# Performance work log

Measured on AMD Instinct MI355X. Metric: run time of the kernel, lower is better.

The kernel has to match this reference:

```python
import jax, jax.numpy as jnp
import numpy as np

B, S, DIM = 2, 4096, 2048
H, HK, HD = 16, 8, 128          # n_heads, n_kv_heads, head_dim
M = 128                          # FAVOR random features (== head_dim)
EPS_FAVOR = 1e-6
EPS_RMS = 1e-5


def _orthogonal_random_matrix(m, d, seed=0):
    # Gaussian orthogonal random features (Performer/FAVOR+), single square block.
    rng = np.random.default_rng(seed)
    a = rng.standard_normal((d, d)).astype(np.float32)
    q, _ = np.linalg.qr(a)
    mat = q.T[:m]
    row_norms = np.linalg.norm(rng.standard_normal((m, d)).astype(np.float32), axis=1)
    return jnp.asarray(mat * row_norms[:, None], dtype=jnp.float32)


def setup_inputs() -> dict:
    key = jax.random.key(0)
    ks = jax.random.split(key, 8)
    hidden_states = jax.random.normal(ks[0], (B, S, DIM), dtype=jnp.float32)
    attention_mask = jax.random.randint(ks[1], (B, S), 0, 2).astype(jnp.int32)
    ang = jax.random.uniform(ks[2], (B, S, HD // 2), dtype=jnp.float32,
                             minval=0.0, maxval=2.0 * np.pi)
    freqs_cis = jnp.stack([jnp.cos(ang), jnp.sin(ang)], axis=-1)  # (B,S,HD/2,2)
    sc = 0.02
    wq = sc * jax.random.normal(ks[3], (H * HD, DIM), dtype=jnp.float32)
    wk = sc * jax.random.normal(ks[4], (HK * HD, DIM), dtype=jnp.float32)
    wv = sc * jax.random.normal(ks[5], (HK * HD, DIM), dtype=jnp.float32)
    wo = sc * jax.random.normal(ks[6], (DIM, H * HD), dtype=jnp.float32)
    gq = jnp.ones((HD,), dtype=jnp.float32)
    gk = jnp.ones((HD,), dtype=jnp.float32)
    proj = _orthogonal_random_matrix(M, HD, seed=0)
    return {"hidden_states": hidden_states, "attention_mask": attention_mask,
            "freqs_cis": freqs_cis, "wq": wq, "wk": wk, "wv": wv, "wo": wo,
            "gq": gq, "gk": gk, "proj": proj}


def _rmsnorm(x, w):
    return x * jax.lax.rsqrt(jnp.mean(x * x, axis=-1, keepdims=True) + EPS_RMS) * w


def _rope(x, fc):
    # x: (B,S,Hx,HD), fc: (B,S,HD/2,2) as (cos, sin); complex mult on pairs.
    xr = x.reshape(*x.shape[:-1], HD // 2, 2)
    a, b = xr[..., 0], xr[..., 1]
    c = fc[:, :, None, :, 0]
    d = fc[:, :, None, :, 1]
    out = jnp.stack([a * c - b * d, a * d + b * c], axis=-1)
    return out.reshape(x.shape)


def _favor_features(x, proj, is_query):
    # x: (B,H,S,D), proj: (M,D) -> positive random features (B,H,S,M)
    d = x.shape[-1]
    x = x * (d ** -0.25)
    xp = jnp.einsum('bhsd,md->bhsm', x, proj)
    xp = xp - 0.5 * jnp.sum(x * x, axis=-1, keepdims=True)
    if is_query:
        xp = xp - jnp.max(xp, axis=-1, keepdims=True)
    else:
        xp = xp - jnp.max(xp, axis=2, keepdims=True)
    return jnp.exp(xp) * (M ** -0.5) + EPS_FAVOR


def reference(hidden_states, attention_mask, freqs_cis, wq, wk, wv, wo, gq, gk, proj):
    x = hidden_states
    q = jnp.einsum('bsd,od->bso', x, wq).reshape(B, S, H, HD)
    k = jnp.einsum('bsd,od->bso', x, wk).reshape(B, S, HK, HD)
    v = jnp.einsum('bsd,od->bso', x, wv).reshape(B, S, HK, HD)
    q = _rmsnorm(q, gq)
    k = _rmsnorm(k, gk)
    q = _rope(q, freqs_cis)
    k = _rope(k, freqs_cis)
    # GQA: expand kv heads (repeat_interleave along head dim)
    rep = H // HK
    k = jnp.repeat(k, rep, axis=2)
    v = jnp.repeat(v, rep, axis=2)
    # (B,H,S,D)
    qh = jnp.transpose(q, (0, 2, 1, 3))
    kh = jnp.transpose(k, (0, 2, 1, 3))
    vh = jnp.transpose(v, (0, 2, 1, 3))
    valid = (attention_mask > 0).astype(jnp.float32)[:, None, :, None]  # (B,1,S,1)
    q_phi = _favor_features(qh, proj, is_query=True)   # (B,H,S,M)
    k_phi = _favor_features(kh, proj, is_query=False)  # (B,H,S,M)
    k_phi = k_phi * valid
    vh = vh * valid
    kv = jnp.einsum('bhsm,bhsd->bhmd', k_phi, vh)      # (B,H,M,D)
    k_sum = jnp.sum(k_phi, axis=2)                     # (B,H,M)
    out = jnp.einsum('bhsm,bhmd->bhsd', q_phi, kv)
    denom = jnp.einsum('bhsm,bhm->bhs', q_phi, k_sum)[..., None]
    out = out / (denom + EPS_FAVOR)
    out = out * valid
    out = jnp.transpose(out, (0, 2, 1, 3)).reshape(B, S, H * HD)
    return jnp.einsum('bso,do->bsd', out, wo)


if __name__ == '__main__':
    o = reference(**setup_inputs())
    print(o.shape, o.dtype)
```

## Files before the change

### kernel.cpp

```cpp
#include <hip/hip_runtime.h>

#define B_ 2
#define S_ 4096
#define DIM_ 2048
#define H_ 16
#define HK_ 8
#define HD_ 128
#define M_ 128

typedef unsigned short u16;
typedef __bf16 bf16x8 __attribute__((ext_vector_type(8)));
typedef float f32x4 __attribute__((ext_vector_type(4)));

__device__ __forceinline__ u16 f2b(float f) {
  unsigned u = __float_as_uint(f);
  u = u + 0x7fffu + ((u >> 16) & 1u);
  return (u16)(u >> 16);
}
__device__ __forceinline__ float b2f(u16 h) {
  return __uint_as_float(((unsigned)h) << 16);
}
__device__ __forceinline__ unsigned fenc(float f) {
  unsigned u = __float_as_uint(f);
  return (u & 0x80000000u) ? ~u : (u | 0x80000000u);
}
__device__ __forceinline__ float fdec(unsigned e) {
  unsigned u = (e & 0x80000000u) ? (e & 0x7fffffffu) : ~e;
  return __uint_as_float(u);
}

__global__ void f2b_kernel(const float* __restrict__ in, u16* __restrict__ out, int n4) {
  int i = blockIdx.x * blockDim.x + threadIdx.x;
  if (i < n4) {
    float4 v = ((const float4*)in)[i];
    ushort4 o;
    o.x = f2b(v.x); o.y = f2b(v.y); o.z = f2b(v.z); o.w = f2b(v.w);
    ((ushort4*)out)[i] = o;
  }
}

__global__ void tproj_kernel(const float* __restrict__ p, float* __restrict__ pT) {
  int i = blockIdx.x * 256 + threadIdx.x;
  int d = i >> 7, m = i & 127;
  pT[i] = p[m * 128 + d];
}

__global__ void init_kernel(float* __restrict__ kvf, unsigned* __restrict__ kmaxu,
                            float* __restrict__ ksum) {
  int i = blockIdx.x * 256 + threadIdx.x;
  if (i < B_ * HK_ * M_ * HD_) kvf[i] = 0.f;
  if (i < B_ * HK_ * M_) { kmaxu[i] = 0u; ksum[i] = 0.f; }
}

__global__ __launch_bounds__(512, 2) void gemm256(
    const u16* __restrict__ A, const u16* __restrict__ Bm, float* __restrict__ C,
    int K, int ldc, int nbx)
{
  __shared__ __align__(16) u16 lds[65536];
  const int t = threadIdx.x;
  const int wave = t >> 6, lane = t & 63;
  const int nwg = gridDim.x;
  const int q8 = nwg >> 3;
  const int id = blockIdx.x;
  const int sid = (id & 7) * q8 + (id >> 3);
  const int nby = nwg / nbx;
  const int by = sid % nby;
  const int bx = sid / nby;
  const int wave_m = wave >> 2;
  const int wave_n = wave & 3;
  const int lr = lane & 15, lg = lane >> 4;

  const int srow = lane >> 3;
  const int scolE = (((lane & 7) ^ srow) << 3);

  const int NT = K >> 6;
  f32x4 acc[8][4] = {};

  const u16* Abase = A + (size_t)bx * 256 * (size_t)K;
  const u16* Bbase = Bm + (size_t)by * 256 * (size_t)K;

#define STAGE256(buf, k0)                                                            \
  {                                                                                  \
    _Pragma("unroll")                                                                \
    for (int sub = 0; sub < 2; sub++) {                                              \
      const int rowH = (wave * 2 + sub) * 8 + srow;                                  \
      const int chunk = (wave * 2 + sub) * 512;                                      \
      _Pragma("unroll")                                                              \
      for (int hh = 0; hh < 2; hh++) {                                               \
        __builtin_amdgcn_global_load_lds(                                            \
            (const __attribute__((address_space(1))) void*)(Abase + (size_t)(hh * 128 + rowH) * K + (k0) + scolE), \
            (__attribute__((address_space(3))) void*)&lds[(buf) * 16384 + hh * 8192 + chunk], 16, 0, 0); \
        __builtin_amdgcn_global_load_lds(                                            \
            (const __attribute__((address_space(1))) void*)(Bbase + (size_t)(hh * 128 + rowH) * K + (k0) + scolE), \
            (__attribute__((address_space(3))) void*)&lds[32768 + (buf) * 16384 + hh * 8192 + chunk], 16, 0, 0); \
      }                                                                              \
    }                                                                                \
  }

  STAGE256(0, 0);
  __syncthreads();

  for (int tt = 0; tt < NT; tt++) {
    const int cur = tt & 1;
    const int AbaseH = cur * 16384 + wave_m * 8192;
    const int BbaseH = 32768 + cur * 16384 + (wave_n >> 1) * 8192;
#pragma unroll
    for (int q = 0; q < 4; q++) {
      if (q == 0 && tt + 1 < NT) { STAGE256(cur ^ 1, (tt + 1) * 64) }
      const int mh = q >> 1, nh = q & 1;
      bf16x8 af[4][2], bfr[2][2];
#pragma unroll
      for (int m = 0; m < 4; m++) {
        const int r = mh * 64 + m * 16 + lr;
#pragma unroll
        for (int kk = 0; kk < 2; kk++) {
          const int cb = ((kk << 6) | (lg << 4)) ^ ((lr & 7) << 4);
          af[m][kk] = *(const bf16x8*)&lds[AbaseH + r * 64 + (cb >> 1)];
        }
      }
#pragma unroll
      for (int n = 0; n < 2; n++) {
        const int r = (wave_n & 1) * 64 + nh * 32 + n * 16 + lr;
#pragma unroll
        for (int kk = 0; kk < 2; kk++) {
          const int cb = ((kk << 6) | (lg << 4)) ^ ((lr & 7) << 4);
          bfr[n][kk] = *(const bf16x8*)&lds[BbaseH + r * 64 + (cb >> 1)];
        }
      }
      asm volatile("" ::: "memory");
      __builtin_amdgcn_s_barrier();
      asm volatile("" ::: "memory");
      __builtin_amdgcn_s_setprio(1);
#pragma unroll
      for (int kk = 0; kk < 2; kk++)
#pragma unroll
        for (int m = 0; m < 4; m++)
#pragma unroll
          for (int n = 0; n < 2; n++)
            acc[mh * 4 + m][nh * 2 + n] =
                __builtin_amdgcn_mfma_f32_16x16x32_bf16(af[m][kk], bfr[n][kk],
                                                        acc[mh * 4 + m][nh * 2 + n], 0, 0, 0);
      __builtin_amdgcn_s_setprio(0);
      asm volatile("" ::: "memory");
      if (q == 3) asm volatile("s_waitcnt vmcnt(0)" ::: "memory");
      __builtin_amdgcn_s_barrier();
      asm volatile("" ::: "memory");
    }
  }

  float* Cb = C + (size_t)(bx * 256 + wave_m * 128 + lg * 4) * ldc + by * 256 + wave_n * 64 + lr;
#pragma unroll
  for (int i = 0; i < 8; i++)
#pragma unroll
    for (int j = 0; j < 4; j++)
#pragma unroll
      for (int r = 0; r < 4; r++)
        Cb[(size_t)(i * 16 + r) * ldc + j * 16] = acc[i][j][r];
#undef STAGE256
}

__global__ __launch_bounds__(256) void gemm_bt(
    const u16* __restrict__ A, const u16* __restrict__ Bm, float* __restrict__ C,
    int M, int N, int K,
    unsigned long long sAb, unsigned long long sBb, unsigned long long sCb,
    int bshiftB, int ldc, int ksplit)
{
  __shared__ __align__(16) u16 sA[128 * 32];
  __shared__ __align__(16) u16 sB[128 * 32];
  const int t = threadIdx.x;
  const int wave = t >> 6, lane = t & 63;
  const int z = blockIdx.z;
  const int batch = z / ksplit;
  const int ks = z - batch * ksplit;
  const int kLen = K / ksplit, kBeg = ks * kLen;

  const u16* Ab = A + (size_t)batch * sAb + (size_t)blockIdx.x * 128 * (size_t)K;
  const u16* Bb = Bm + (size_t)(batch >> bshiftB) * sBb + (size_t)blockIdx.y * 128 * (size_t)K;
  float* Cb = C + (size_t)batch * sCb + (size_t)blockIdx.x * 128 * (size_t)ldc
                + (size_t)blockIdx.y * 128;

  const int r0 = wave * 16 + (lane >> 2);
  const int e0 = (lane & 3) * 8;
  const int wr = wave >> 1, wc = wave & 1;

  f32x4 acc[4][4] = {};

  for (int k0 = kBeg; k0 < kBeg + kLen; k0 += 32) {
#pragma unroll
    for (int i = 0; i < 2; i++) {
      __builtin_amdgcn_global_load_lds(
          (const __attribute__((address_space(1))) void*)(Ab + (size_t)(r0 + i * 64) * K + k0 + e0),
          (__attribute__((address_space(3))) void*)(&sA[(i * 4 + wave) * 512]), 16, 0, 0);
      __builtin_amdgcn_global_load_lds(
          (const __attribute__((address_space(1))) void*)(Bb + (size_t)(r0 + i * 64) * K + k0 + e0),
          (__attribute__((address_space(3))) void*)(&sB[(i * 4 + wave) * 512]), 16, 0, 0);
    }
    __syncthreads();
    bf16x8 av[4], bv[4];
#pragma unroll
    for (int m = 0; m < 4; m++)
      av[m] = *(const bf16x8*)&sA[(wr * 64 + m * 16 + (lane & 15)) * 32 + (lane >> 4) * 8];
#pragma unroll
    for (int n = 0; n < 4; n++)
      bv[n] = *(const bf16x8*)&sB[(wc * 64 + n * 16 + (lane & 15)) * 32 + (lane >> 4) * 8];
#pragma unroll
    for (int m = 0; m < 4; m++)
#pragma unroll
      for (int n = 0; n < 4; n++)
        acc[m][n] = __builtin_amdgcn_mfma_f32_16x16x32_bf16(av[m], bv[n], acc[m][n], 0, 0, 0);
    __syncthreads();
  }

  const int crow0 = wr * 64 + (lane >> 4) * 4;
  const int ccol = wc * 64 + (lane & 15);
  if (ksplit == 1) {
#pragma unroll
    for (int m = 0; m < 4; m++)
#pragma unroll
      for (int n = 0; n < 4; n++)
#pragma unroll
        for (int r = 0; r < 4; r++)
          Cb[(size_t)(crow0 + m * 16 + r) * ldc + ccol + n * 16] = acc[m][n][r];
  } else {
#pragma unroll
    for (int m = 0; m < 4; m++)
#pragma unroll
      for (int n = 0; n < 4; n++)
#pragma unroll
        for (int r = 0; r < 4; r++)
          atomicAdd(&Cb[(size_t)(crow0 + m * 16 + r) * ldc + ccol + n * 16], acc[m][n][r]);
  }
}

__global__ __launch_bounds__(256) void gemm_out_epi(
    const u16* __restrict__ qphib, const u16* __restrict__ kvb,
    const float* __restrict__ denom, const int* __restrict__ amask,
    u16* __restrict__ attnb)
{
  __shared__ __align__(16) u16 sA[128 * 32];
  __shared__ __align__(16) u16 sB[128 * 32];
  const int t = threadIdx.x;
  const int wave = t >> 6, lane = t & 63;
  const int batch = blockIdx.z;
  const int b = batch >> 4, h = batch & 15;

  const u16* Ab = qphib + (size_t)batch * 524288 + (size_t)blockIdx.x * 128 * 128;
  const u16* Bb = kvb + (size_t)(batch >> 1) * 16384;

  const int r0 = wave * 16 + (lane >> 2);
  const int e0 = (lane & 3) * 8;
  const int wr = wave >> 1, wc = wave & 1;

  f32x4 acc[4][4] = {};

  for (int k0 = 0; k0 < 128; k0 += 32) {
#pragma unroll
    for (int i = 0; i < 2; i++) {
      __builtin_amdgcn_global_load_lds(
          (const __attribute__((address_space(1))) void*)(Ab + (size_t)(r0 + i * 64) * 128 + k0 + e0),
          (__attribute__((address_space(3))) void*)(&sA[(i * 4 + wave) * 512]), 16, 0, 0);
      __builtin_amdgcn_global_load_lds(
          (const __attribute__((address_space(1))) void*)(Bb + (size_t)(r0 + i * 64) * 128 + k0 + e0),
          (__attribute__((address_space(3))) void*)(&sB[(i * 4 + wave) * 512]), 16, 0, 0);
    }
    __syncthreads();
    bf16x8 av[4], bv[4];
#pragma unroll
    for (int m = 0; m < 4; m++)
      av[m] = *(const bf16x8*)&sA[(wr * 64 + m * 16 + (lane & 15)) * 32 + (lane >> 4) * 8];
#pragma unroll
    for (int n = 0; n < 4; n++)
      bv[n] = *(const bf16x8*)&sB[(wc * 64 + n * 16 + (lane & 15)) * 32 + (lane >> 4) * 8];
#pragma unroll
    for (int m = 0; m < 4; m++)
#pragma unroll
      for (int n = 0; n < 4; n++)
        acc[m][n] = __builtin_amdgcn_mfma_f32_16x16x32_bf16(av[m], bv[n], acc[m][n], 0, 0, 0);
    __syncthreads();
  }

  const int crow0 = wr * 64 + (lane >> 4) * 4;
  const int ccol = wc * 64 + (lane & 15);
#pragma unroll
  for (int m = 0; m < 4; m++)
#pragma unroll
    for (int r = 0; r < 4; r++) {
      const int s = blockIdx.x * 128 + crow0 + m * 16 + r;
      const float inv = (amask[b * S_ + s] > 0)
                          ? 1.f / (denom[(size_t)batch * S_ + s] + 1e-6f) : 0.f;
      u16* orow = attnb + ((size_t)(b * S_ + s)) * 2048 + h * 128 + ccol;
#pragma unroll
      for (int n = 0; n < 4; n++)
        orow[n * 16] = f2b(acc[m][n][r] * inv);
    }
}

template <int IS_Q>
__global__ __launch_bounds__(256) void favor_kernel(
    const float* __restrict__ qkv, const float* __restrict__ fc,
    const float* __restrict__ g, const float* __restrict__ pT,
    float* __restrict__ kpre, unsigned* __restrict__ kmaxu,
    u16* __restrict__ qphib, const float* __restrict__ ksum, float* __restrict__ denom,
    int colbase)
{
  const int b = blockIdx.z, h = blockIdx.y;
  const int wave = threadIdx.x >> 6, lane = threadIdx.x & 63;
  const int s0 = blockIdx.x * 16 + wave * 4;
  __shared__ float xs[4][4][128];
  __shared__ float sm[4][128];
  float halfss[4];
  const int col = colbase + h * HD_;

#pragma unroll
  for (int tt = 0; tt < 4; tt++) {
    const int s = s0 + tt;
    const size_t row = (size_t)b * S_ + s;
    const float* xr = qkv + row * 4096 + col;
    float a = xr[2 * lane], bb = xr[2 * lane + 1];
    float ss = a * a + bb * bb;
#pragma unroll
    for (int o = 1; o < 64; o <<= 1) ss += __shfl_xor(ss, o);
    const float sc = rsqrtf(ss * (1.f / HD_) + 1e-5f);
    a *= sc * g[2 * lane];
    bb *= sc * g[2 * lane + 1];
    const float2 cs = *(const float2*)&fc[(row * 64 + lane) * 2];
    float na = a * cs.x - bb * cs.y;
    float nb = a * cs.y + bb * cs.x;
    na *= 0.29730177875068026f;
    nb *= 0.29730177875068026f;
    xs[wave][tt][2 * lane] = na;
    xs[wave][tt][2 * lane + 1] = nb;
    float s2 = na * na + nb * nb;
#pragma unroll
    for (int o = 1; o < 64; o <<= 1) s2 += __shfl_xor(s2, o);
    halfss[tt] = 0.5f * s2;
  }

  float acc[4][2] = {};
  for (int d = 0; d < 128; d++) {
    const float2 p = *(const float2*)&pT[d * 128 + 2 * lane];
#pragma unroll
    for (int tt = 0; tt < 4; tt++) {
      const float xv = xs[wave][tt][d];
      acc[tt][0] = fmaf(p.x, xv, acc[tt][0]);
      acc[tt][1] = fmaf(p.y, xv, acc[tt][1]);
    }
  }

  if (IS_Q) {
#pragma unroll
    for (int tt = 0; tt < 4; tt++) {
      const int s = s0 + tt;
      const float p0 = acc[tt][0] - halfss[tt], p1 = acc[tt][1] - halfss[tt];
      float mx = fmaxf(p0, p1);
#pragma unroll
      for (int o = 1; o < 64; o <<= 1) mx = fmaxf(mx, __shfl_xor(mx, o));
      const float f0 = expf(p0 - mx) * 0.08838834764831845f + 1e-6f;
      const float f1 = expf(p1 - mx) * 0.08838834764831845f + 1e-6f;
      const u16 u0 = f2b(f0), u1 = f2b(f1);
      const size_t base = (((size_t)(b * H_ + h)) * S_ + s) * M_;
      ushort2 st2; st2.x = u0; st2.y = u1;
      *(ushort2*)&qphib[base + 2 * lane] = st2;
      const float* ksb = ksum + ((b * HK_) + (h >> 1)) * M_;
      float dsum = b2f(u0) * ksb[2 * lane] + b2f(u1) * ksb[2 * lane + 1];
#pragma unroll
      for (int o = 1; o < 64; o <<= 1) dsum += __shfl_xor(dsum, o);
      if (lane == 0) denom[((size_t)(b * H_ + h)) * S_ + s] = dsum;
    }
  } else {
    float mx0 = -1e30f, mx1 = -1e30f;
#pragma unroll
    for (int tt = 0; tt < 4; tt++) {
      const int s = s0 + tt;
      const float p0 = acc[tt][0] - halfss[tt], p1 = acc[tt][1] - halfss[tt];
      const size_t base = (((size_t)(b * HK_ + h)) * S_ + s) * M_;
      float2 w2; w2.x = p0; w2.y = p1;
      *(float2*)&kpre[base + 2 * lane] = w2;
      mx0 = fmaxf(mx0, p0);
      mx1 = fmaxf(mx1, p1);
    }
    sm[wave][2 * lane] = mx0;
    sm[wave][2 * lane + 1] = mx1;
    __syncthreads();
    if (threadIdx.x < 128) {
      const float v = fmaxf(fmaxf(sm[0][threadIdx.x], sm[1][threadIdx.x]),
                            fmaxf(sm[2][threadIdx.x], sm[3][threadIdx.x]));
      atomicMax(&kmaxu[(b * HK_ + h) * M_ + threadIdx.x], fenc(v));
    }
  }
}

__global__ __launch_bounds__(256) void kexp_kernel(
    const float* __restrict__ kpre, const unsigned* __restrict__ kmaxu,
    const int* __restrict__ amask, u16* __restrict__ kphiT, float* __restrict__ ksum)
{
  const int b = blockIdx.z, hk = blockIdx.y;
  const int c0 = blockIdx.x * 64;
  const int t = threadIdx.x;
  const int m = t & 127, half = t >> 7;
  __shared__ __align__(16) u16 st[128][64];
  __shared__ float red[256];
  const int bhk = b * HK_ + hk;
  const float kmax = fdec(kmaxu[bhk * M_ + m]);
  float sum = 0.f;
  const int msw = (m & 7) << 3;
  for (int i = 0; i < 32; i++) {
    const int sl = half * 32 + i;
    const int s = c0 + sl;
    const float pre = kpre[(((size_t)bhk) * S_ + s) * M_ + m];
    const int va = amask[b * S_ + s] > 0;
    const float phi = va ? (expf(pre - kmax) * 0.08838834764831845f + 1e-6f) : 0.f;
    sum += phi;
    st[m][sl ^ msw] = f2b(phi);
  }
  red[t] = sum;
  __syncthreads();
  if (t < 128) atomicAdd(&ksum[bhk * M_ + t], red[t] + red[t + 128]);
  const int mr = t >> 1, part = t & 1;
  const int rsw = (mr & 7) << 3;
  const size_t base = ((size_t)(bhk * M_ + mr)) * S_ + c0 + part * 32;
#pragma unroll
  for (int k = 0; k < 4; k++)
    *(uint4*)&kphiT[base + k * 8] = *(const uint4*)&st[mr][(part * 32 + k * 8) ^ rsw];
}

__global__ __launch_bounds__(256) void vT_kernel(
    const float* __restrict__ qkv, const int* __restrict__ amask, u16* __restrict__ vT)
{
  const int b = blockIdx.z, hk = blockIdx.y;
  const int c0 = blockIdx.x * 64;
  const int t = threadIdx.x;
  const int d = t & 127, half = t >> 7;
  __shared__ __align__(16) u16 st[128][64];
  const int bhk = b * HK_ + hk;
  const int dsw = (d & 7) << 3;
  for (int i = 0; i < 32; i++) {
    const int sl = half * 32 + i;
    const int s = c0 + sl;
    const float v = qkv[((size_t)(b * S_ + s)) * 4096 + 3072 + hk * 128 + d];
    const int va = amask[b * S_ + s] > 0;
    st[d][sl ^ dsw] = f2b(va ? v : 0.f);
  }
  __syncthreads();
  const int dr = t >> 1, part = t & 1;
  const int rsw = (dr & 7) << 3;
  const size_t base = ((size_t)(bhk * 128 + dr)) * S_ + c0 + part * 32;
#pragma unroll
  for (int k = 0; k < 4; k++)
    *(uint4*)&vT[base + k * 8] = *(const uint4*)&st[dr][(part * 32 + k * 8) ^ rsw];
}

__global__ void kvb_kernel(const float* __restrict__ kvf, u16* __restrict__ kvb) {
  const int i = blockIdx.x * 256 + threadIdx.x;
  const int bhk = i >> 14;
  const int rem = i & 16383;
  const int d = rem >> 7, m = rem & 127;
  kvb[i] = f2b(kvf[(bhk << 14) + m * 128 + d]);
}

extern "C" void kernel_launch(void* const* d_in, const int* in_sizes, int n_in,
                              void* d_out, int out_size, void* d_ws, size_t ws_size,
                              hipStream_t stream)
{
  const float* x  = (const float*)d_in[0];
  const int*   am = (const int*)d_in[1];
  const float* fc = (const float*)d_in[2];
  const float* wq = (const float*)d_in[3];
  const float* wk = (const float*)d_in[4];
  const float* wv = (const float*)d_in[5];
  const float* wo = (const float*)d_in[6];
  const float* gq = (const float*)d_in[7];
  const float* gk = (const float*)d_in[8];
  const float* pj = (const float*)d_in[9];
  float* out = (float*)d_out;

  char* w = (char*)d_ws;
  size_t off = 0;
  u16*   xb    = (u16*)(w + off);  off += (size_t)B_ * S_ * DIM_ * 2;
  u16*   wqkvb = (u16*)(w + off);  off += 4096ull * 2048 * 2;
  u16*   wob   = (u16*)(w + off);  off += 2048ull * 2048 * 2;
  float* qkv   = (float*)(w + off); off += (size_t)B_ * S_ * 4096 * 4;
  float* kpre  = (float*)(w + off); off += (size_t)B_ * HK_ * S_ * M_ * 4;
  u16*   kphiT = (u16*)(w + off);  off += (size_t)B_ * HK_ * S_ * M_ * 2;
  u16*   vT    = (u16*)(w + off);  off += (size_t)B_ * HK_ * S_ * HD_ * 2;
  float* kvf   = (float*)(w + off); off += (size_t)B_ * HK_ * M_ * HD_ * 4;
  u16*   kvb   = (u16*)(w + off);  off += (size_t)B_ * HK_ * M_ * HD_ * 2;
  float* pT    = (float*)(w + off); off += 128ull * 128 * 4;
  unsigned* kmaxu = (unsigned*)(w + off); off += (size_t)B_ * HK_ * M_ * 4;
  float* ksum  = (float*)(w + off); off += (size_t)B_ * HK_ * M_ * 4;
  float* denom = (float*)(w + off); off += (size_t)B_ * H_ * S_ * 4;
  u16*   attnb = xb;
  u16*   qphib = (u16*)kpre;
  if (ws_size < off) return;

  f2b_kernel<<<16384, 256, 0, stream>>>(x, xb, 4194304);
  f2b_kernel<<<4096, 256, 0, stream>>>(wq, wqkvb, 1048576);
  f2b_kernel<<<2048, 256, 0, stream>>>(wk, wqkvb + 4194304, 524288);
  f2b_kernel<<<2048, 256, 0, stream>>>(wv, wqkvb + 6291456, 524288);
  f2b_kernel<<<4096, 256, 0, stream>>>(wo, wob, 1048576);
  tproj_kernel<<<64, 256, 0, stream>>>(pj, pT);
  init_kernel<<<1024, 256, 0, stream>>>(kvf, kmaxu, ksum);

  gemm256<<<512, 512, 0, stream>>>(xb, wqkvb, qkv, 2048, 4096, 32);

  favor_kernel<0><<<dim3(S_ / 16, HK_, B_), 256, 0, stream>>>(
      qkv, fc, gk, pT, kpre, kmaxu, nullptr, nullptr, nullptr, 2048);
  kexp_kernel<<<dim3(S_ / 64, HK_, B_), 256, 0, stream>>>(kpre, kmaxu, am, kphiT, ksum);
  vT_kernel<<<dim3(S_ / 64, HK_, B_), 256, 0, stream>>>(qkv, am, vT);
  favor_kernel<1><<<dim3(S_ / 16, H_, B_), 256, 0, stream>>>(
      qkv, fc, gq, pT, nullptr, nullptr, qphib, ksum, denom, 0);

  gemm_bt<<<dim3(1, 1, 256), 256, 0, stream>>>(kphiT, vT, kvf,
      128, 128, 4096, 524288ull, 524288ull, 16384ull, 0, 128, 16);
  kvb_kernel<<<1024, 256, 0, stream>>>(kvf, kvb);

  gemm_out_epi<<<dim3(32, 1, 32), 256, 0, stream>>>(qphib, kvb, denom, am, attnb);

  gemm256<<<256, 512, 0, stream>>>(attnb, wob, out, 2048, 2048, 32);
}
```

Measured before the change: 694.4 us.

## Fuse prep launches and spread gemm256 prefetch across four phases

Merges the five bf16 conversion launches, the projection transpose and the accumulator init into one prep kernel, removing launch gaps between small kernels. In gemm256, next-tile global-to-LDS loads are split into four quarter stages issued one per MFMA phase, with partial vmcnt waits instead of one full drain at the end of each tile. This spreads memory traffic over the compute phases but makes the wait-count and barrier ordering harder to get right.

```diff
diff --git a/kernel.cpp b/kernel.cpp
--- a/kernel.cpp
+++ b/kernel.cpp
@@ -12,6 +12,9 @@
 typedef __bf16 bf16x8 __attribute__((ext_vector_type(8)));
 typedef float f32x4 __attribute__((ext_vector_type(4)));
 
+#define AS1 __attribute__((address_space(1)))
+#define AS3 __attribute__((address_space(3)))
+
 __device__ __forceinline__ u16 f2b(float f) {
   unsigned u = __float_as_uint(f);
   u = u + 0x7fffu + ((u >> 16) & 1u);
@@ -29,27 +32,67 @@
   return __uint_as_float(u);
 }
 
-__global__ void f2b_kernel(const float* __restrict__ in, u16* __restrict__ out, int n4) {
-  int i = blockIdx.x * blockDim.x + threadIdx.x;
-  if (i < n4) {
-    float4 v = ((const float4*)in)[i];
-    ushort4 o;
-    o.x = f2b(v.x); o.y = f2b(v.y); o.z = f2b(v.z); o.w = f2b(v.w);
-    ((ushort4*)out)[i] = o;
-  }
-}
-
-__global__ void tproj_kernel(const float* __restrict__ p, float* __restrict__ pT) {
-  int i = blockIdx.x * 256 + threadIdx.x;
-  int d = i >> 7, m = i & 127;
-  pT[i] = p[m * 128 + d];
-}
-
-__global__ void init_kernel(float* __restrict__ kvf, unsigned* __restrict__ kmaxu,
-                            float* __restrict__ ksum) {
-  int i = blockIdx.x * 256 + threadIdx.x;
-  if (i < B_ * HK_ * M_ * HD_) kvf[i] = 0.f;
-  if (i < B_ * HK_ * M_) { kmaxu[i] = 0u; ksum[i] = 0.f; }
+__global__ __launch_bounds__(256) void prep_kernel(
+    const float* __restrict__ x, const float* __restrict__ wq,
+    const float* __restrict__ wk, const float* __restrict__ wv,
+    const float* __restrict__ wo, const float* __restrict__ pj,
+    u16* __restrict__ xb, u16* __restrict__ wqkvb, u16* __restrict__ wob,
+    float* __restrict__ pT, float* __restrict__ kvf,
+    unsigned* __restrict__ kmaxu, float* __restrict__ ksum)
+{
+  int bid = blockIdx.x;
+  const int t = threadIdx.x;
+  if (bid < 16384) {
+    const int i = bid * 256 + t;
+    float4 v = ((const float4*)x)[i];
+    ushort4 o; o.x = f2b(v.x); o.y = f2b(v.y); o.z = f2b(v.z); o.w = f2b(v.w);
+    ((ushort4*)xb)[i] = o;
+    return;
+  }
+  bid -= 16384;
+  if (bid < 4096) {
+    const int i = bid * 256 + t;
+    float4 v = ((const float4*)wq)[i];
+    ushort4 o; o.x = f2b(v.x); o.y = f2b(v.y); o.z = f2b(v.z); o.w = f2b(v.w);
+    ((ushort4*)wqkvb)[i] = o;
+    return;
+  }
+  bid -= 4096;
+  if (bid < 2048) {
+    const int i = bid * 256 + t;
+    float4 v = ((const float4*)wk)[i];
+    ushort4 o; o.x = f2b(v.x); o.y = f2b(v.y); o.z = f2b(v.z); o.w = f2b(v.w);
+    ((ushort4*)(wqkvb + 4194304))[i] = o;
+    return;
+  }
+  bid -= 2048;
+  if (bid < 2048) {
+    const int i = bid * 256 + t;
+    float4 v = ((const float4*)wv)[i];
+    ushort4 o; o.x = f2b(v.x); o.y = f2b(v.y); o.z = f2b(v.z); o.w = f2b(v.w);
+    ((ushort4*)(wqkvb + 6291456))[i] = o;
+    return;
+  }
+  bid -= 2048;
+  if (bid < 4096) {
+    const int i = bid * 256 + t;
+    float4 v = ((const float4*)wo)[i];
+    ushort4 o; o.x = f2b(v.x); o.y = f2b(v.y); o.z = f2b(v.z); o.w = f2b(v.w);
+    ((ushort4*)wob)[i] = o;
+    return;
+  }
+  bid -= 4096;
+  if (bid < 64) {
+    const int i = bid * 256 + t;
+    pT[i] = pj[(i & 127) * 128 + (i >> 7)];
+    return;
+  }
+  bid -= 64;
+  {
+    const int i = bid * 256 + t;
+    if (i < B_ * HK_ * M_ * HD_) kvf[i] = 0.f;
+    if (i < B_ * HK_ * M_) { kmaxu[i] = 0u; ksum[i] = 0.f; }
+  }
 }
 
 __global__ __launch_bounds__(512, 2) void gemm256(
@@ -79,73 +122,90 @@
   const u16* Abase = A + (size_t)bx * 256 * (size_t)K;
   const u16* Bbase = Bm + (size_t)by * 256 * (size_t)K;
 
-#define STAGE256(buf, k0)                                                            \
-  {                                                                                  \
-    _Pragma("unroll")                                                                \
-    for (int sub = 0; sub < 2; sub++) {                                              \
-      const int rowH = (wave * 2 + sub) * 8 + srow;                                  \
-      const int chunk = (wave * 2 + sub) * 512;                                      \
-      _Pragma("unroll")                                                              \
-      for (int hh = 0; hh < 2; hh++) {                                               \
-        __builtin_amdgcn_global_load_lds(                                            \
-            (const __attribute__((address_space(1))) void*)(Abase + (size_t)(hh * 128 + rowH) * K + (k0) + scolE), \
-            (__attribute__((address_space(3))) void*)&lds[(buf) * 16384 + hh * 8192 + chunk], 16, 0, 0); \
-        __builtin_amdgcn_global_load_lds(                                            \
-            (const __attribute__((address_space(1))) void*)(Bbase + (size_t)(hh * 128 + rowH) * K + (k0) + scolE), \
-            (__attribute__((address_space(3))) void*)&lds[32768 + (buf) * 16384 + hh * 8192 + chunk], 16, 0, 0); \
-      }                                                                              \
-    }                                                                                \
-  }
-
-  STAGE256(0, 0);
-  __syncthreads();
-
-  for (int tt = 0; tt < NT; tt++) {
-    const int cur = tt & 1;
+#define STAGE_B(sub, nb, kn)                                                          \
+  {                                                                                   \
+    _Pragma("unroll")                                                                 \
+    for (int hh = 0; hh < 2; hh++)                                                    \
+      __builtin_amdgcn_global_load_lds(                                               \
+          (const AS1 void*)(Bbase + (size_t)(hh * 128 + (wave * 2 + (sub)) * 8 + srow) * K + (kn) + scolE), \
+          (AS3 void*)&lds[32768 + (nb) * 16384 + hh * 8192 + (wave * 2 + (sub)) * 512], 16, 0, 0); \
+  }
+#define STAGE_AE(nb, kn)                                                              \
+  {                                                                                   \
+    _Pragma("unroll")                                                                 \
+    for (int hh = 0; hh < 2; hh++)                                                    \
+      __builtin_amdgcn_global_load_lds(                                               \
+          (const AS1 void*)(Abase + (size_t)(hh * 128 + wave * 8 + srow) * K + (kn) + scolE), \
+          (AS3 void*)&lds[(nb) * 16384 + hh * 8192 + wave * 512], 16, 0, 0);          \
+  }
+#define STAGE_AL(nb, kn)                                                              \
+  {                                                                                   \
+    _Pragma("unroll")                                                                 \
+    for (int hh = 0; hh < 2; hh++)                                                    \
+      __builtin_amdgcn_global_load_lds(                                               \
+          (const AS1 void*)(Abase + (size_t)(hh * 128 + 64 + wave * 8 + srow) * K + (kn) + scolE), \
+          (AS3 void*)&lds[(nb) * 16384 + hh * 8192 + (8 + wave) * 512], 16, 0, 0);    \
+  }
+
+#define DO_PHASE(mh, nh, STAGE_STMT, PRE_BAR_WAIT)                                    \
+  {                                                                                   \
+    bf16x8 af[4][2], bv[2][2];                                                        \
+    _Pragma("unroll")                                                                 \
+    for (int m = 0; m < 4; m++) {                                                     \
+      const int r = (mh) * 64 + m * 16 + lr;                                          \
+      _Pragma("unroll")                                                               \
+      for (int kk = 0; kk < 2; kk++) {                                                \
+        const int cb = ((kk << 6) | (lg << 4)) ^ ((lr & 7) << 4);                     \
+        af[m][kk] = *(const bf16x8*)&lds[AbaseH + r * 64 + (cb >> 1)];                \
+      }                                                                               \
+    }                                                                                 \
+    _Pragma("unroll")                                                                 \
+    for (int n = 0; n < 2; n++) {                                                     \
+      const int r = (wave_n & 1) * 64 + (nh) * 32 + n * 16 + lr;                      \
+      _Pragma("unroll")                                                               \
+      for (int kk = 0; kk < 2; kk++) {                                                \
+        const int cb = ((kk << 6) | (lg << 4)) ^ ((lr & 7) << 4);                     \
+        bv[n][kk] = *(const bf16x8*)&lds[BbaseH + r * 64 + (cb >> 1)];                \
+      }                                                                               \
+    }                                                                                 \
+    STAGE_STMT;                                                                       \
+    asm volatile("" ::: "memory");                                                    \
+    __builtin_amdgcn_s_barrier();                                                     \
+    asm volatile("" ::: "memory");                                                    \
+    __builtin_amdgcn_s_setprio(1);                                                    \
+    _Pragma("unroll")                                                                 \
+    for (int kk = 0; kk < 2; kk++)                                                    \
+      _Pragma("unroll")                                                               \
+      for (int m = 0; m < 4; m++)                                                     \
+        _Pragma("unroll")                                                             \
+        for (int n = 0; n < 2; n++)                                                   \
+          acc[(mh) * 4 + m][(nh) * 2 + n] = __builtin_amdgcn_mfma_f32_16x16x32_bf16(  \
+              af[m][kk], bv[n][kk], acc[(mh) * 4 + m][(nh) * 2 + n], 0, 0, 0);        \
+    __builtin_amdgcn_s_setprio(0);                                                    \
+    PRE_BAR_WAIT;                                                                     \
+    asm volatile("" ::: "memory");                                                    \
+    __builtin_amdgcn_s_barrier();                                                     \
+    asm volatile("" ::: "memory");                                                    \
+  }
+
+  STAGE_B(0, 0, 0) STAGE_B(1, 0, 0) STAGE_AE(0, 0) STAGE_AL(0, 0)
+  asm volatile("s_waitcnt vmcnt(2)" ::: "memory");
+  __builtin_amdgcn_s_barrier();
+  asm volatile("" ::: "memory");
+
+  for (int tt = 0; tt < NT; ++tt) {
+    const int cur = tt & 1, nxt = cur ^ 1;
+    const int kn = (tt + 1) << 6;
+    const bool nl = (tt + 1 < NT);
     const int AbaseH = cur * 16384 + wave_m * 8192;
     const int BbaseH = 32768 + cur * 16384 + (wave_n >> 1) * 8192;
-#pragma unroll
-    for (int q = 0; q < 4; q++) {
-      if (q == 0 && tt + 1 < NT) { STAGE256(cur ^ 1, (tt + 1) * 64) }
-      const int mh = q >> 1, nh = q & 1;
-      bf16x8 af[4][2], bfr[2][2];
-#pragma unroll
-      for (int m = 0; m < 4; m++) {
-        const int r = mh * 64 + m * 16 + lr;
-#pragma unroll
-        for (int kk = 0; kk < 2; kk++) {
-          const int cb = ((kk << 6) | (lg << 4)) ^ ((lr & 7) << 4);
-          af[m][kk] = *(const bf16x8*)&lds[AbaseH + r * 64 + (cb >> 1)];
-        }
-      }
-#pragma unroll
-      for (int n = 0; n < 2; n++) {
-        const int r = (wave_n & 1) * 64 + nh * 32 + n * 16 + lr;
-#pragma unroll
-        for (int kk = 0; kk < 2; kk++) {
-          const int cb = ((kk << 6) | (lg << 4)) ^ ((lr & 7) << 4);
-          bfr[n][kk] = *(const bf16x8*)&lds[BbaseH + r * 64 + (cb >> 1)];
-        }
-      }
-      asm volatile("" ::: "memory");
-      __builtin_amdgcn_s_barrier();
-      asm volatile("" ::: "memory");
-      __builtin_amdgcn_s_setprio(1);
-#pragma unroll
-      for (int kk = 0; kk < 2; kk++)
-#pragma unroll
-        for (int m = 0; m < 4; m++)
-#pragma unroll
-          for (int n = 0; n < 2; n++)
-            acc[mh * 4 + m][nh * 2 + n] =
-                __builtin_amdgcn_mfma_f32_16x16x32_bf16(af[m][kk], bfr[n][kk],
-                                                        acc[mh * 4 + m][nh * 2 + n], 0, 0, 0);
-      __builtin_amdgcn_s_setprio(0);
-      asm volatile("" ::: "memory");
-      if (q == 3) asm volatile("s_waitcnt vmcnt(0)" ::: "memory");
-      __builtin_amdgcn_s_barrier();
-      asm volatile("" ::: "memory");
-    }
+    DO_PHASE(0, 0, if (nl) { STAGE_B(0, nxt, kn) }, )
+    DO_PHASE(0, 1, if (nl) { STAGE_B(1, nxt, kn) },
+             if (nl) { asm volatile("s_waitcnt vmcnt(4)" ::: "memory"); }
+             else    { asm volatile("s_waitcnt vmcnt(0)" ::: "memory"); })
+    DO_PHASE(1, 0, if (nl) { STAGE_AE(nxt, kn) }, )
+    DO_PHASE(1, 1, if (nl) { STAGE_AL(nxt, kn) },
+             asm volatile("s_waitcnt vmcnt(2)" ::: "memory");)
   }
 
   float* Cb = C + (size_t)(bx * 256 + wave_m * 128 + lg * 4) * ldc + by * 256 + wave_n * 64 + lr;
@@ -156,7 +216,10 @@
 #pragma unroll
       for (int r = 0; r < 4; r++)
         Cb[(size_t)(i * 16 + r) * ldc + j * 16] = acc[i][j][r];
-#undef STAGE256
+#undef DO_PHASE
+#undef STAGE_B
+#undef STAGE_AE
+#undef STAGE_AL
 }
 
 __global__ __launch_bounds__(256) void gemm_bt(
@@ -189,11 +252,11 @@
 #pragma unroll
     for (int i = 0; i < 2; i++) {
       __builtin_amdgcn_global_load_lds(
-          (const __attribute__((address_space(1))) void*)(Ab + (size_t)(r0 + i * 64) * K + k0 + e0),
-          (__attribute__((address_space(3))) void*)(&sA[(i * 4 + wave) * 512]), 16, 0, 0);
+          (const AS1 void*)(Ab + (size_t)(r0 + i * 64) * K + k0 + e0),
+          (AS3 void*)(&sA[(i * 4 + wave) * 512]), 16, 0, 0);
       __builtin_amdgcn_global_load_lds(
-          (const __attribute__((address_space(1))) void*)(Bb + (size_t)(r0 + i * 64) * K + k0 + e0),
-          (__attribute__((address_space(3))) void*)(&sB[(i * 4 + wave) * 512]), 16, 0, 0);
+          (const AS1 void*)(Bb + (size_t)(r0 + i * 64) * K + k0 + e0),
+          (AS3 void*)(&sB[(i * 4 + wave) * 512]), 16, 0, 0);
     }
     __syncthreads();
     bf16x8 av[4], bv[4];
@@ -257,11 +320,11 @@
 #pragma unroll
     for (int i = 0; i < 2; i++) {
       __builtin_amdgcn_global_load_lds(
-          (const __attribute__((address_space(1))) void*)(Ab + (size_t)(r0 + i * 64) * 128 + k0 + e0),
-          (__attribute__((address_space(3))) void*)(&sA[(i * 4 + wave) * 512]), 16, 0, 0);
+          (const AS1 void*)(Ab + (size_t)(r0 + i * 64) * 128 + k0 + e0),
+          (AS3 void*)(&sA[(i * 4 + wave) * 512]), 16, 0, 0);
       __builtin_amdgcn_global_load_lds(
-          (const __attribute__((address_space(1))) void*)(Bb + (size_t)(r0 + i * 64) * 128 + k0 + e0),
-          (__attribute__((address_space(3))) void*)(&sB[(i * 4 + wave) * 512]), 16, 0, 0);
+          (const AS1 void*)(Bb + (size_t)(r0 + i * 64) * 128 + k0 + e0),
+          (AS3 void*)(&sB[(i * 4 + wave) * 512]), 16, 0, 0);
     }
     __syncthreads();
     bf16x8 av[4], bv[4];
@@ -493,13 +556,8 @@
   u16*   qphib = (u16*)kpre;
   if (ws_size < off) return;
 
-  f2b_kernel<<<16384, 256, 0, stream>>>(x, xb, 4194304);
-  f2b_kernel<<<4096, 256, 0, stream>>>(wq, wqkvb, 1048576);
-  f2b_kernel<<<2048, 256, 0, stream>>>(wk, wqkvb + 4194304, 524288);
-  f2b_kernel<<<2048, 256, 0, stream>>>(wv, wqkvb + 6291456, 524288);
-  f2b_kernel<<<4096, 256, 0, stream>>>(wo, wob, 1048576);
-  tproj_kernel<<<64, 256, 0, stream>>>(pj, pT);
-  init_kernel<<<1024, 256, 0, stream>>>(kvf, kmaxu, ksum);
+  prep_kernel<<<29760, 256, 0, stream>>>(x, wq, wk, wv, wo, pj,
+                                         xb, wqkvb, wob, pT, kvf, kmaxu, ksum);
 
   gemm256<<<512, 512, 0, stream>>>(xb, wqkvb, qkv, 2048, 4096, 32);
 
```

Result: faster. 668.7 us (-3.7%).
